# Performance work log

Measured on AMD Instinct MI355X. Metric: run time of the kernel, lower is better.

The kernel has to match this reference:

```python
import jax, jax.numpy as jnp
import numpy as np

# dims: L=tgt len, S=src len, N=batch, E=embed, H=heads
L, S, N, E, H = 1024, 1024, 4, 1024, 16
HD = E // H  # head dim = 64


def setup_inputs() -> dict:
    key = jax.random.key(0)
    ks = jax.random.split(key, 7)
    w_scale = 0.02
    return {
        "query": jax.random.normal(ks[0], (L, N, E), jnp.float32),
        "key": jax.random.normal(ks[1], (S, N, E), jnp.float32),
        "value": jax.random.normal(ks[2], (S, N, E), jnp.float32),
        "in_proj_weight": jax.random.normal(ks[3], (3 * E, E), jnp.float32) * w_scale,
        "in_proj_bias": jax.random.normal(ks[4], (3 * E,), jnp.float32) * w_scale,
        "out_proj_weight": jax.random.normal(ks[5], (E, E), jnp.float32) * w_scale,
        "out_proj_bias": jax.random.normal(ks[6], (E,), jnp.float32) * w_scale,
    }


def reference(query, key, value, in_proj_weight, in_proj_bias,
              out_proj_weight, out_proj_bias):
    scaling = float(HD) ** -0.5
    # packed QKV projection, sliced exactly as the torch code does
    q = (query @ in_proj_weight[:E].T + in_proj_bias[:E]) * scaling        # (L,N,E)
    k = key @ in_proj_weight[E:2 * E].T + in_proj_bias[E:2 * E]            # (S,N,E)
    v = value @ in_proj_weight[2 * E:].T + in_proj_bias[2 * E:]            # (S,N,E)
    # split heads: (L,N,E) -> (N*H, L, HD)
    q = q.reshape(L, N * H, HD).transpose(1, 0, 2)
    k = k.reshape(S, N * H, HD).transpose(1, 0, 2)
    v = v.reshape(S, N * H, HD).transpose(1, 0, 2)
    scores = jnp.einsum('bld,bsd->bls', q, k)          # (N*H, L, S)
    attn = jax.nn.softmax(scores, axis=-1)
    sig = jax.nn.sigmoid(scores)                        # the need_sigmoid_weights variant
    out = jnp.einsum('bls,bsd->bld', attn, v)          # (N*H, L, HD)
    out = out.transpose(1, 0, 2).reshape(L, N, E)
    out = out @ out_proj_weight.T + out_proj_bias       # (L,N,E)
    # weights averaged over heads, as torch MHA returns: (N,L,S)
    attn_weights = attn.reshape(N, H, L, S).sum(axis=1) / H
    sig_weights = sig.reshape(N, H, L, S).sum(axis=1) / H
    return out, attn_weights, sig_weights
```

## Files before the change

### kernel.cpp

```cpp
#include <hip/hip_runtime.h>

#define L_DIM 1024
#define E_DIM 1024
#define NB 4
#define H_NUM 16
#define HD_DIM 64
#define T_TOK 4096
#define NHB 64

typedef float f32x4 __attribute__((ext_vector_type(4)));
typedef unsigned short u16x8 __attribute__((ext_vector_type(8)));
typedef unsigned short u16x4 __attribute__((ext_vector_type(4)));
typedef __bf16 bf16x8 __attribute__((ext_vector_type(8)));

__device__ inline unsigned short f2bf(float f) {
  unsigned int u = __builtin_bit_cast(unsigned int, f);
  u += 0x7FFFu + ((u >> 16) & 1u);
  return (unsigned short)(u >> 16);
}
__device__ inline f32x4 mfma16(u16x8 a, u16x8 b, f32x4 c) {
  return __builtin_amdgcn_mfma_f32_16x16x32_bf16(
      __builtin_bit_cast(bf16x8, a), __builtin_bit_cast(bf16x8, b), c, 0, 0, 0);
}

__device__ __forceinline__ void gl2lds16(const void* g, void* l) {
  auto gp = reinterpret_cast<const __attribute__((address_space(1))) unsigned int*>(
      reinterpret_cast<unsigned long long>(g));
  auto lp = reinterpret_cast<__attribute__((address_space(3))) unsigned int*>(
      static_cast<unsigned int>(reinterpret_cast<unsigned long long>(l)));
  __builtin_amdgcn_global_load_lds(gp, lp, 16, 0, 0);
}

__global__ __launch_bounds__(256) void cast_kernel(
    const float* __restrict__ s0, const float* __restrict__ s1,
    const float* __restrict__ s2, const float* __restrict__ s3,
    unsigned short* __restrict__ d0, unsigned short* __restrict__ d1,
    unsigned short* __restrict__ d2, unsigned short* __restrict__ d3,
    int n0, int n1, int n2, int n3) {
  const int y = blockIdx.y;
  const float* s = (y == 0) ? s0 : (y == 1) ? s1 : (y == 2) ? s2 : s3;
  unsigned short* d = (y == 0) ? d0 : (y == 1) ? d1 : (y == 2) ? d2 : d3;
  const int n = (y == 0) ? n0 : (y == 1) ? n1 : (y == 2) ? n2 : n3;
  int idx = (blockIdx.x * 256 + threadIdx.x) * 8;
  const int stride = gridDim.x * 256 * 8;
  for (; idx < n; idx += stride) {
    float4 a = *(const float4*)(s + idx);
    float4 b = *(const float4*)(s + idx + 4);
    u16x8 o = {f2bf(a.x), f2bf(a.y), f2bf(a.z), f2bf(a.w),
               f2bf(b.x), f2bf(b.y), f2bf(b.z), f2bf(b.w)};
    *(u16x8*)(d + idx) = o;
  }
}

__device__ __forceinline__ void stage_tile(const unsigned short* __restrict__ g,
                                           unsigned short* lbuf, int tid) {
  const int r = tid >> 2, c = tid & 3;
  const int sc = c ^ ((r ^ (r >> 2)) & 3);
  gl2lds16(g + (size_t)r * 1024 + sc * 8, lbuf + tid * 8);
  const int r2 = r + 64;
  gl2lds16(g + (size_t)r2 * 1024 + sc * 8, lbuf + (tid + 256) * 8);
}
__device__ __forceinline__ int frag_off(int r, int q) {
  return r * 32 + ((q ^ ((r ^ (r >> 2)) & 3)) << 3);
}

__global__ __launch_bounds__(256) void qkv_gemm(
    const unsigned short* __restrict__ qb, const unsigned short* __restrict__ kb,
    const unsigned short* __restrict__ vb, const unsigned short* __restrict__ Wb,
    const float* __restrict__ bias, unsigned short* __restrict__ q_hm,
    unsigned short* __restrict__ k_hm, unsigned short* __restrict__ v_t) {
  __shared__ __align__(16) unsigned short As[2][4096];
  __shared__ __align__(16) unsigned short Bs[2][4096];
  const int tid = threadIdx.x;
  const int bm = blockIdx.x, bn = blockIdx.y, z = blockIdx.z;
  const unsigned short* Ag = ((z == 0) ? qb : (z == 1) ? kb : vb) + (size_t)bm * 128 * 1024;
  const unsigned short* Bg = Wb + (size_t)z * 1048576 + (size_t)bn * 128 * 1024;
  const float* bc = bias + z * E_DIM;

  const int w = tid >> 6, lane = tid & 63;
  const int wm = w & 1, wn = w >> 1;
  const int quad = lane >> 4, l16 = lane & 15;

  f32x4 acc[4][4];
#pragma unroll
  for (int i = 0; i < 4; i++)
#pragma unroll
    for (int j = 0; j < 4; j++) { f32x4 zz = {0.f, 0.f, 0.f, 0.f}; acc[i][j] = zz; }

  stage_tile(Ag, As[0], tid);
  stage_tile(Bg, Bs[0], tid);

  for (int kk = 0; kk < 32; kk++) {
    __syncthreads();
    if (kk + 1 < 32) {
      const int bf = (kk + 1) & 1;
      stage_tile(Ag + (kk + 1) * 32, As[bf], tid);
      stage_tile(Bg + (kk + 1) * 32, Bs[bf], tid);
    }
    const int cb = kk & 1;
    u16x8 af[4], bfv[4];
#pragma unroll
    for (int mi = 0; mi < 4; mi++) {
      int r = wm * 64 + mi * 16 + l16;
      af[mi] = *(const u16x8*)&As[cb][frag_off(r, quad)];
    }
#pragma unroll
    for (int ni = 0; ni < 4; ni++) {
      int r = wn * 64 + ni * 16 + l16;
      bfv[ni] = *(const u16x8*)&Bs[cb][frag_off(r, quad)];
    }
#pragma unroll
    for (int mi = 0; mi < 4; mi++)
#pragma unroll
      for (int ni = 0; ni < 4; ni++)
        acc[mi][ni] = mfma16(af[mi], bfv[ni], acc[mi][ni]);
  }
#pragma unroll
  for (int ni = 0; ni < 4; ni++) {
    int col = bn * 128 + wn * 64 + ni * 16 + l16;
    float bv = bc[col];
    int h = col >> 6, d = col & 63;
#pragma unroll
    for (int mi = 0; mi < 4; mi++) {
#pragma unroll
      for (int r = 0; r < 4; r++) {
        int t = bm * 128 + wm * 64 + mi * 16 + quad * 4 + r;
        float v = acc[mi][ni][r] + bv;
        int nb = t & 3, pos = t >> 2;
        if (z == 0) {
          v *= 0.125f;
          q_hm[(size_t)((nb * 16 + h) * 1024 + pos) * 64 + d] = f2bf(v);
        } else if (z == 1) {
          k_hm[(size_t)((nb * 16 + h) * 1024 + pos) * 64 + d] = f2bf(v);
        } else {
          v_t[(size_t)((nb * 16 + h) * 64 + d) * 1024 + pos] = f2bf(v);
        }
      }
    }
  }
}

__global__ __launch_bounds__(256, 2) void attn_kernel(
    const unsigned short* __restrict__ q_hm, const unsigned short* __restrict__ k_hm,
    const unsigned short* __restrict__ v_t, unsigned short* __restrict__ o_h,
    float* __restrict__ m_ws, float* __restrict__ r_ws) {
  __shared__ __align__(16) unsigned short stage[8][4096];
  __shared__ __align__(16) unsigned short pt[2][32][68];
  __shared__ float red_m[4][32];
  __shared__ float red_s[4][32];

  const int tid = threadIdx.x;
  const int flat = blockIdx.x + (blockIdx.y << 5);
  const int nf = (flat & 7) * 256 + (flat >> 3);
  const int l0 = (nf & 31) * 32;
  const int b = nf >> 5;
  const int nb = b >> 4, h = b & 15;
  const int w = tid >> 6, lane = tid & 63;
  const int quad = lane >> 4, l16 = lane & 15;

  const int i1 = tid + 256;
  const int r0s = tid >> 3, c0s = tid & 7;
  const int r1s = i1 >> 3, c1s = i1 & 7;
  const int src0 = (c0s ^ (r0s & 7)) * 8;
  const int src1 = (c1s ^ (r1s & 7)) * 8;

  const unsigned short* kbase = k_hm + ((size_t)b << 16);
  const unsigned short* vbase = v_t + ((size_t)b << 16);

  u16x8 bq[2][2];
#pragma unroll
  for (int g = 0; g < 2; g++) {
    const unsigned short* qp =
        q_hm + ((size_t)(b * 1024 + l0 + g * 16 + l16) << 6) + quad * 8;
    bq[g][0] = *(const u16x8*)qp;
    bq[g][1] = *(const u16x8*)(qp + 32);
  }
  asm volatile("" ::: "memory");

  f32x4 acc[16][2];
#pragma unroll
  for (int j = 0; j < 16; j++)
#pragma unroll
    for (int g = 0; g < 2; g++) { f32x4 z = {0.f, 0.f, 0.f, 0.f}; acc[j][g] = z; }

#pragma unroll
  for (int t = 0; t < 3; t++) {
    gl2lds16(kbase + ((size_t)(t * 64 + r0s) << 6) + src0, &stage[t][tid * 8]);
    gl2lds16(kbase + ((size_t)(t * 64 + r1s) << 6) + src1, &stage[t][i1 * 8]);
  }

  const int myrow = w * 16 + l16;
  const int sw0 = ((quad ^ (l16 & 7)) * 8);
  const int sw1 = (((quad + 4) ^ (l16 & 7)) * 8);

#pragma unroll
  for (int j = 0; j < 16; j++) {
    if (j + 3 < 16) {
      gl2lds16(kbase + ((size_t)((j + 3) * 64 + r0s) << 6) + src0,
               &stage[(j + 3) & 7][tid * 8]);
      gl2lds16(kbase + ((size_t)((j + 3) * 64 + r1s) << 6) + src1,
               &stage[(j + 3) & 7][i1 * 8]);
    } else {
      const int vt = j + 3 - 16;
      gl2lds16(vbase + ((size_t)r0s << 10) + vt * 64 + src0,
               &stage[(j + 3) & 7][tid * 8]);
      gl2lds16(vbase + ((size_t)r1s << 10) + vt * 64 + src1,
               &stage[(j + 3) & 7][i1 * 8]);
    }
    asm volatile("s_waitcnt vmcnt(6)" ::: "memory");
    __builtin_amdgcn_s_barrier();
    asm volatile("" ::: "memory");
    const unsigned short* kt = &stage[j & 7][myrow * 64];
    u16x8 ak0 = *(const u16x8*)(kt + sw0);
    u16x8 ak1 = *(const u16x8*)(kt + sw1);
    acc[j][0] = mfma16(ak0, bq[0][0], acc[j][0]);
    acc[j][0] = mfma16(ak1, bq[0][1], acc[j][0]);
    acc[j][1] = mfma16(ak0, bq[1][0], acc[j][1]);
    acc[j][1] = mfma16(ak1, bq[1][1], acc[j][1]);
  }

  float lm0 = -3e38f, lm1 = -3e38f;
#pragma unroll
  for (int j = 0; j < 16; j++)
#pragma unroll
    for (int r = 0; r < 4; r++) {
      lm0 = fmaxf(lm0, acc[j][0][r]);
      lm1 = fmaxf(lm1, acc[j][1][r]);
    }
  lm0 = fmaxf(lm0, __shfl_xor(lm0, 16, 64));
  lm0 = fmaxf(lm0, __shfl_xor(lm0, 32, 64));
  lm1 = fmaxf(lm1, __shfl_xor(lm1, 16, 64));
  lm1 = fmaxf(lm1, __shfl_xor(lm1, 32, 64));
  if (lane < 16) { red_m[w][lane] = lm0; red_m[w][lane + 16] = lm1; }
  asm volatile("s_waitcnt lgkmcnt(0)" ::: "memory");
  __builtin_amdgcn_s_barrier();
  asm volatile("" ::: "memory");
  float m0 = fmaxf(fmaxf(red_m[0][l16], red_m[1][l16]),
                   fmaxf(red_m[2][l16], red_m[3][l16]));
  float m1 = fmaxf(fmaxf(red_m[0][l16 + 16], red_m[1][l16 + 16]),
                   fmaxf(red_m[2][l16 + 16], red_m[3][l16 + 16]));
  float mm = 0.f;
  if (tid < 32)
    mm = fmaxf(fmaxf(red_m[0][tid], red_m[1][tid]),
               fmaxf(red_m[2][tid], red_m[3][tid]));

  float ls0 = 0.f, ls1 = 0.f;
#pragma unroll
  for (int j = 0; j < 16; j++) {
#pragma unroll
    for (int r = 0; r < 4; r++) {
      float e0 = __expf(acc[j][0][r] - m0);
      float e1 = __expf(acc[j][1][r] - m1);
      acc[j][0][r] = e0;
      acc[j][1][r] = e1;
      ls0 += e0;
      ls1 += e1;
    }
  }
  ls0 += __shfl_xor(ls0, 16, 64);
  ls0 += __shfl_xor(ls0, 32, 64);
  ls1 += __shfl_xor(ls1, 16, 64);
  ls1 += __shfl_xor(ls1, 32, 64);
  if (lane < 16) { red_s[w][lane] = ls0; red_s[w][lane + 16] = ls1; }
  asm volatile("s_waitcnt lgkmcnt(0)" ::: "memory");
  __builtin_amdgcn_s_barrier();
  asm volatile("" ::: "memory");
  float rv0 = 1.0f / (red_s[0][l16] + red_s[1][l16] + red_s[2][l16] + red_s[3][l16]);
  float rv1 = 1.0f / (red_s[0][l16 + 16] + red_s[1][l16 + 16] +
                      red_s[2][l16 + 16] + red_s[3][l16 + 16]);
  float ssv = 1.f;
  if (tid < 32)
    ssv = red_s[0][tid] + red_s[1][tid] + red_s[2][tid] + red_s[3][tid];

  {
    u16x4 p0 = {f2bf(acc[0][0][0]), f2bf(acc[0][0][1]), f2bf(acc[0][0][2]), f2bf(acc[0][0][3])};
    u16x4 p1 = {f2bf(acc[0][1][0]), f2bf(acc[0][1][1]), f2bf(acc[0][1][2]), f2bf(acc[0][1][3])};
    *(u16x4*)&pt[0][l16][w * 16 + quad * 4] = p0;
    *(u16x4*)&pt[0][16 + l16][w * 16 + quad * 4] = p1;
  }

  f32x4 oacc0 = {0.f, 0.f, 0.f, 0.f};
  f32x4 oacc1 = {0.f, 0.f, 0.f, 0.f};
#pragma unroll
  for (int j = 0; j < 16; j++) {
    if (j < 13) {
      const int t = j + 3;
      gl2lds16(vbase + ((size_t)r0s << 10) + t * 64 + src0, &stage[t & 7][tid * 8]);
      gl2lds16(vbase + ((size_t)r1s << 10) + t * 64 + src1, &stage[t & 7][i1 * 8]);
      asm volatile("s_waitcnt vmcnt(6) lgkmcnt(0)" ::: "memory");
    } else if (j == 13) {
      asm volatile("s_waitcnt vmcnt(4) lgkmcnt(0)" ::: "memory");
    } else if (j == 14) {
      asm volatile("s_waitcnt vmcnt(2) lgkmcnt(0)" ::: "memory");
    } else {
      asm volatile("s_waitcnt vmcnt(0) lgkmcnt(0)" ::: "memory");
    }
    __builtin_amdgcn_s_barrier();
    asm volatile("" ::: "memory");
    if (j < 15) {
      const int bf = (j + 1) & 1;
      u16x4 p0 = {f2bf(acc[j + 1][0][0]), f2bf(acc[j + 1][0][1]),
                  f2bf(acc[j + 1][0][2]), f2bf(acc[j + 1][0][3])};
      u16x4 p1 = {f2bf(acc[j + 1][1][0]), f2bf(acc[j + 1][1][1]),
                  f2bf(acc[j + 1][1][2]), f2bf(acc[j + 1][1][3])};
      *(u16x4*)&pt[bf][l16][w * 16 + quad * 4] = p0;
      *(u16x4*)&pt[bf][16 + l16][w * 16 + quad * 4] = p1;
    }
    const unsigned short* vt = &stage[j & 7][myrow * 64];
    u16x8 bv0 = *(const u16x8*)(vt + sw0);
    u16x8 bv1 = *(const u16x8*)(vt + sw1);
    u16x8 ap00 = *(const u16x8*)&pt[j & 1][l16][quad * 8];
    u16x8 ap01 = *(const u16x8*)&pt[j & 1][l16][32 + quad * 8];
    u16x8 ap10 = *(const u16x8*)&pt[j & 1][16 + l16][quad * 8];
    u16x8 ap11 = *(const u16x8*)&pt[j & 1][16 + l16][32 + quad * 8];
    oacc0 = mfma16(ap00, bv0, oacc0);
    oacc0 = mfma16(ap01, bv1, oacc0);
    oacc1 = mfma16(ap10, bv0, oacc1);
    oacc1 = mfma16(ap11, bv1, oacc1);
  }

  if (tid < 32) {
    m_ws[b * 1024 + l0 + tid] = mm;
    r_ws[b * 1024 + l0 + tid] = 1.0f / ssv;
  }

#pragma unroll
  for (int r = 0; r < 4; r++) {
    int lr = quad * 4 + r;
    float rr0 = __shfl(rv0, lr, 64);
    float rr1 = __shfl(rv1, lr, 64);
    int t0 = (l0 + lr) * 4 + nb;
    int t1 = (l0 + 16 + lr) * 4 + nb;
    o_h[((size_t)t0 << 10) + h * 64 + w * 16 + l16] = f2bf(oacc0[r] * rr0);
    o_h[((size_t)t1 << 10) + h * 64 + w * 16 + l16] = f2bf(oacc1[r] * rr1);
  }
}

__global__ __launch_bounds__(256) void weights_kernel(
    const unsigned short* __restrict__ q_hm, const unsigned short* __restrict__ k_hm,
    const float* __restrict__ m_ws, const float* __restrict__ r_ws,
    float* __restrict__ attn_out, float* __restrict__ sig_out) {
  __shared__ __align__(16) unsigned short qs[2][4096];
  __shared__ __align__(16) unsigned short ks[2][4096];
  __shared__ float ml[16][64];
  __shared__ float rl[16][64];
  __shared__ float cl[16][64];

  const int tid = threadIdx.x;
  const int s0 = blockIdx.x * 64;
  const int l0 = blockIdx.y * 64;
  const int nb = blockIdx.z;
  const int w = tid >> 6, lane = tid & 63;
  const int quad = lane >> 4, l16 = lane & 15;

  const int i1 = tid + 256;
  const int r0s = tid >> 3, c0s = tid & 7;
  const int r1s = i1 >> 3, c1s = i1 & 7;
  const int src0 = (c0s ^ (r0s & 7)) * 8;
  const int src1 = (c1s ^ (r1s & 7)) * 8;

  {
    int idx = tid * 4;
    int hh = idx >> 6, ii = idx & 63;
    int bb = nb * 16 + hh;
    float4 mv4 = *(const float4*)&m_ws[bb * 1024 + l0 + ii];
    float4 rv4 = *(const float4*)&r_ws[bb * 1024 + l0 + ii];
    *(float4*)&ml[hh][ii] = mv4;
    *(float4*)&rl[hh][ii] = rv4;
    float4 cv4 = {__expf(-mv4.x), __expf(-mv4.y), __expf(-mv4.z), __expf(-mv4.w)};
    *(float4*)&cl[hh][ii] = cv4;
  }

  {
    int bb = nb * 16;
    const unsigned short* qb = q_hm + ((size_t)(bb * 1024 + l0) << 6);
    const unsigned short* kb = k_hm + ((size_t)(bb * 1024 + s0) << 6);
    gl2lds16(qb + (r0s << 6) + src0, &qs[0][tid * 8]);
    gl2lds16(qb + (r1s << 6) + src1, &qs[0][i1 * 8]);
    gl2lds16(kb + (r0s << 6) + src0, &ks[0][tid * 8]);
    gl2lds16(kb + (r1s << 6) + src1, &ks[0][i1 * 8]);
  }

  const int sw0 = ((quad ^ (l16 & 7)) * 8);
  const int sw1 = (((quad + 4) ^ (l16 & 7)) * 8);

  f32x4 accA[4], accS[4];
#pragma unroll
  for (int i = 0; i < 4; i++) {
    f32x4 zz = {0.f, 0.f, 0.f, 0.f};
    accA[i] = zz; accS[i] = zz;
  }

#pragma unroll
  for (int h = 0; h < 16; h++) {
    __syncthreads();
    if (h + 1 < 16) {
      int bf = (h + 1) & 1;
      int bb = nb * 16 + h + 1;
      const unsigned short* qb = q_hm + ((size_t)(bb * 1024 + l0) << 6);
      const unsigned short* kb = k_hm + ((size_t)(bb * 1024 + s0) << 6);
      gl2lds16(qb + (r0s << 6) + src0, &qs[bf][tid * 8]);
      gl2lds16(qb + (r1s << 6) + src1, &qs[bf][i1 * 8]);
      gl2lds16(kb + (r0s << 6) + src0, &ks[bf][tid * 8]);
      gl2lds16(kb + (r1s << 6) + src1, &ks[bf][i1 * 8]);
    }
    const int bf = h & 1;
    const unsigned short* qt = &qs[bf][(w * 16 + l16) * 64];
    u16x8 a0 = *(const u16x8*)(qt + sw0);
    u16x8 a1 = *(const u16x8*)(qt + sw1);
    f32x4 mv = *(const f32x4*)&ml[h][w * 16 + quad * 4];
    f32x4 rv = *(const f32x4*)&rl[h][w * 16 + quad * 4];
    f32x4 cv = *(const f32x4*)&cl[h][w * 16 + quad * 4];
#pragma unroll
    for (int ni = 0; ni < 4; ni++) {
      const unsigned short* kt = &ks[bf][(ni * 16 + l16) * 64];
      u16x8 b0 = *(const u16x8*)(kt + sw0);
      u16x8 b1 = *(const u16x8*)(kt + sw1);
      f32x4 scv = {0.f, 0.f, 0.f, 0.f};
      scv = mfma16(a0, b0, scv);
      scv = mfma16(a1, b1, scv);
#pragma unroll
      for (int r = 0; r < 4; r++) {
        float e = __expf(scv[r] - mv[r]);
        accA[ni][r] += e * rv[r];
        accS[ni][r] += e * __builtin_amdgcn_rcpf(e + cv[r]);
      }
    }
  }
  const float inv_h = 1.0f / 16.0f;
  const int lrow0 = l0 + w * 16;
#pragma unroll
  for (int ni = 0; ni < 4; ni++) {
#pragma unroll
    for (int r = 0; r < 4; r++) {
      int l = lrow0 + quad * 4 + r;
      int s = s0 + ni * 16 + l16;
      size_t idx = ((size_t)nb * 1024 + l) * 1024 + s;
      attn_out[idx] = accA[ni][r] * inv_h;
      sig_out[idx] = accS[ni][r] * inv_h;
    }
  }
}

__global__ __launch_bounds__(256) void out_gemm(
    const unsigned short* __restrict__ o_h, const unsigned short* __restrict__ Wb,
    const float* __restrict__ bias, float* __restrict__ out) {
  __shared__ __align__(16) unsigned short As[2][4096];
  __shared__ __align__(16) unsigned short Bs[2][4096];
  const int tid = threadIdx.x;
  const int bm = blockIdx.x, bn = blockIdx.y;
  const unsigned short* Ag = o_h + (size_t)bm * 128 * 1024;
  const unsigned short* Bg = Wb + (size_t)bn * 128 * 1024;

  const int w = tid >> 6, lane = tid & 63;
  const int wm = w & 1, wn = w >> 1;
  const int quad = lane >> 4, l16 = lane & 15;

  f32x4 acc[4][4];
#pragma unroll
  for (int i = 0; i < 4; i++)
#pragma unroll
    for (int j = 0; j < 4; j++) { f32x4 zz = {0.f, 0.f, 0.f, 0.f}; acc[i][j] = zz; }

  stage_tile(Ag, As[0], tid);
  stage_tile(Bg, Bs[0], tid);

  for (int kk = 0; kk < 32; kk++) {
    __syncthreads();
    if (kk + 1 < 32) {
      const int bf = (kk + 1) & 1;
      stage_tile(Ag + (kk + 1) * 32, As[bf], tid);
      stage_tile(Bg + (kk + 1) * 32, Bs[bf], tid);
    }
    const int cb = kk & 1;
    u16x8 af[4], bfv[4];
#pragma unroll
    for (int mi = 0; mi < 4; mi++) {
      int r = wm * 64 + mi * 16 + l16;
      af[mi] = *(const u16x8*)&As[cb][frag_off(r, quad)];
    }
#pragma unroll
    for (int ni = 0; ni < 4; ni++) {
      int r = wn * 64 + ni * 16 + l16;
      bfv[ni] = *(const u16x8*)&Bs[cb][frag_off(r, quad)];
    }
#pragma unroll
    for (int mi = 0; mi < 4; mi++)
#pragma unroll
      for (int ni = 0; ni < 4; ni++)
        acc[mi][ni] = mfma16(af[mi], bfv[ni], acc[mi][ni]);
  }
#pragma unroll
  for (int ni = 0; ni < 4; ni++) {
    int col = bn * 128 + wn * 64 + ni * 16 + l16;
    float bv = bias[col];
#pragma unroll
    for (int mi = 0; mi < 4; mi++) {
#pragma unroll
      for (int r = 0; r < 4; r++) {
        int t = bm * 128 + wm * 64 + mi * 16 + quad * 4 + r;
        out[(size_t)t * E_DIM + col] = acc[mi][ni][r] + bv;
      }
    }
  }
}

extern "C" void kernel_launch(void* const* d_in, const int* in_sizes, int n_in,
                              void* d_out, int out_size, void* d_ws, size_t ws_size,
                              hipStream_t stream) {
  const float* qin  = (const float*)d_in[0];
  const float* kin  = (const float*)d_in[1];
  const float* vin  = (const float*)d_in[2];
  const float* Wqkv = (const float*)d_in[3];
  const float* bqkv = (const float*)d_in[4];
  const float* Wout = (const float*)d_in[5];
  const float* bout = (const float*)d_in[6];
  float* out      = (float*)d_out;
  float* attn_out = out + 4194304;
  float* sig_out  = out + 8388608;

  unsigned short* q_hm = (unsigned short*)d_ws;
  unsigned short* k_hm = q_hm + 4194304;
  unsigned short* v_t  = q_hm + 8388608;
  unsigned short* o_h  = q_hm + 12582912;
  float* m_ws = (float*)(q_hm + 16777216);
  float* r_ws = m_ws + 65536;

  unsigned short* qb = (unsigned short*)(out + 4194304);
  unsigned short* kb = qb + 4194304;
  unsigned short* vb = qb + 8388608;
  unsigned short* Wqkvb = o_h;
  unsigned short* Woutb = v_t;

  cast_kernel<<<dim3(2048, 4), 256, 0, stream>>>(
      qin, kin, vin, Wqkv, qb, kb, vb, Wqkvb,
      4194304, 4194304, 4194304, 3145728);
  qkv_gemm<<<dim3(32, 8, 3), 256, 0, stream>>>(qb, kb, vb, Wqkvb, bqkv,
                                               q_hm, k_hm, v_t);
  attn_kernel<<<dim3(32, 64), 256, 0, stream>>>(q_hm, k_hm, v_t, o_h, m_ws, r_ws);
  cast_kernel<<<dim3(512, 1), 256, 0, stream>>>(
      Wout, Wout, Wout, Wout, Woutb, Woutb, Woutb, Woutb,
      1048576, 0, 0, 0);
  weights_kernel<<<dim3(16, 16, 4), 256, 0, stream>>>(q_hm, k_hm, m_ws, r_ws,
                                                      attn_out, sig_out);
  out_gemm<<<dim3(32, 8), 256, 0, stream>>>(o_h, Woutb, bout, out);
}
```

Baseline: 276.3 us.

## Deepen weights_kernel Q/K prefetch to a 4-buffer pipeline and remap blocks per XCD

The head loop in weights_kernel now uses four LDS buffers and stages Q/K two heads ahead. It replaces the full __syncthreads per iteration with explicit vmcnt waits plus a raw s_barrier, so more global-to-LDS loads stay in flight while MFMA/exp work runs. Block indices are also remapped so each XCD handles one batch's tiles, which improves L2 reuse of the shared Q/K data, and launch_bounds now requests 2 blocks per CU. The cost is doubled LDS per block (about 44KB), which may limit occupancy. The hand-written waitcnt counts must exactly match the loads issued per stage, or reads may race with incoming data.

```diff
diff --git a/kernel.cpp b/kernel.cpp
--- a/kernel.cpp
+++ b/kernel.cpp
@@ -336,20 +336,24 @@
   }
 }
 
-__global__ __launch_bounds__(256) void weights_kernel(
+__global__ __launch_bounds__(256, 2) void weights_kernel(
     const unsigned short* __restrict__ q_hm, const unsigned short* __restrict__ k_hm,
     const float* __restrict__ m_ws, const float* __restrict__ r_ws,
     float* __restrict__ attn_out, float* __restrict__ sig_out) {
-  __shared__ __align__(16) unsigned short qs[2][4096];
-  __shared__ __align__(16) unsigned short ks[2][4096];
+  __shared__ __align__(16) unsigned short qs[4][4096];
+  __shared__ __align__(16) unsigned short ks[4][4096];
   __shared__ float ml[16][64];
   __shared__ float rl[16][64];
   __shared__ float cl[16][64];
 
   const int tid = threadIdx.x;
-  const int s0 = blockIdx.x * 64;
-  const int l0 = blockIdx.y * 64;
-  const int nb = blockIdx.z;
+  const int flat = blockIdx.x + (blockIdx.y << 4) + (blockIdx.z << 8);
+  const int xcd = flat & 7, local = flat >> 3;
+  const int nb = xcd >> 1;
+  const int idx2 = ((xcd & 1) << 7) + local;
+  const int l0 = (idx2 >> 4) << 6;
+  const int s0 = (idx2 & 15) << 6;
+
   const int w = tid >> 6, lane = tid & 63;
   const int quad = lane >> 4, l16 = lane & 15;
 
@@ -371,18 +375,19 @@
     *(float4*)&cl[hh][ii] = cv4;
   }
 
-  {
-    int bb = nb * 16;
+  const int sw0 = ((quad ^ (l16 & 7)) * 8);
+  const int sw1 = (((quad + 4) ^ (l16 & 7)) * 8);
+
+  auto stageQK = [&](int h) {
+    const int bb = nb * 16 + h;
     const unsigned short* qb = q_hm + ((size_t)(bb * 1024 + l0) << 6);
     const unsigned short* kb = k_hm + ((size_t)(bb * 1024 + s0) << 6);
-    gl2lds16(qb + (r0s << 6) + src0, &qs[0][tid * 8]);
-    gl2lds16(qb + (r1s << 6) + src1, &qs[0][i1 * 8]);
-    gl2lds16(kb + (r0s << 6) + src0, &ks[0][tid * 8]);
-    gl2lds16(kb + (r1s << 6) + src1, &ks[0][i1 * 8]);
-  }
-
-  const int sw0 = ((quad ^ (l16 & 7)) * 8);
-  const int sw1 = (((quad + 4) ^ (l16 & 7)) * 8);
+    const int bf = h & 3;
+    gl2lds16(qb + (r0s << 6) + src0, &qs[bf][tid * 8]);
+    gl2lds16(qb + (r1s << 6) + src1, &qs[bf][i1 * 8]);
+    gl2lds16(kb + (r0s << 6) + src0, &ks[bf][tid * 8]);
+    gl2lds16(kb + (r1s << 6) + src1, &ks[bf][i1 * 8]);
+  };
 
   f32x4 accA[4], accS[4];
 #pragma unroll
@@ -391,20 +396,12 @@
     accA[i] = zz; accS[i] = zz;
   }
 
-#pragma unroll
-  for (int h = 0; h < 16; h++) {
-    __syncthreads();
-    if (h + 1 < 16) {
-      int bf = (h + 1) & 1;
-      int bb = nb * 16 + h + 1;
-      const unsigned short* qb = q_hm + ((size_t)(bb * 1024 + l0) << 6);
-      const unsigned short* kb = k_hm + ((size_t)(bb * 1024 + s0) << 6);
-      gl2lds16(qb + (r0s << 6) + src0, &qs[bf][tid * 8]);
-      gl2lds16(qb + (r1s << 6) + src1, &qs[bf][i1 * 8]);
-      gl2lds16(kb + (r0s << 6) + src0, &ks[bf][tid * 8]);
-      gl2lds16(kb + (r1s << 6) + src1, &ks[bf][i1 * 8]);
-    }
-    const int bf = h & 1;
+  stageQK(0);
+  stageQK(1);
+  asm volatile("s_waitcnt lgkmcnt(0)" ::: "memory");
+
+  auto computeH = [&](int h) {
+    const int bf = h & 3;
     const unsigned short* qt = &qs[bf][(w * 16 + l16) * 64];
     u16x8 a0 = *(const u16x8*)(qt + sw0);
     u16x8 a1 = *(const u16x8*)(qt + sw1);
@@ -426,7 +423,25 @@
         accS[ni][r] += e * __builtin_amdgcn_rcpf(e + cv[r]);
       }
     }
-  }
+  };
+
+#pragma unroll 1
+  for (int h = 0; h < 14; ++h) {
+    stageQK(h + 2);
+    asm volatile("s_waitcnt vmcnt(8)" ::: "memory");
+    __builtin_amdgcn_s_barrier();
+    asm volatile("" ::: "memory");
+    computeH(h);
+  }
+  asm volatile("s_waitcnt vmcnt(4)" ::: "memory");
+  __builtin_amdgcn_s_barrier();
+  asm volatile("" ::: "memory");
+  computeH(14);
+  asm volatile("s_waitcnt vmcnt(0)" ::: "memory");
+  __builtin_amdgcn_s_barrier();
+  asm volatile("" ::: "memory");
+  computeH(15);
+
   const float inv_h = 1.0f / 16.0f;
   const int lrow0 = l0 + w * 16;
 #pragma unroll
```

Measured after the change: 252.2 us. 1.1x faster.
